# Performance work log

Measured on AMD Instinct MI355X. Metric: run time of the kernel, lower is better.

Reference implementation:

```python
import jax, jax.numpy as jnp
import numpy as np

B, S, D = 2, 2048, 1024
H = 16
HD = D // H  # 64

def setup_inputs() -> dict:
    key = jax.random.key(0)
    k1, k2, k3 = jax.random.split(key, 3)
    scale = 0.02
    return {
        "x": jax.random.normal(k1, (B, S, D), dtype=jnp.float32),
        "w_qkv": jax.random.normal(k2, (D, 3 * D), dtype=jnp.float32) * scale,
        "b_qkv": jnp.zeros((3 * D,), dtype=jnp.float32),
        "w_proj": jax.random.normal(k3, (D, D), dtype=jnp.float32) * scale,
        "b_proj": jnp.zeros((D,), dtype=jnp.float32),
    }

def reference(x, w_qkv, b_qkv, w_proj, b_proj):
    batch, seq_len, _ = x.shape
    qkv = x @ w_qkv + b_qkv                      # [B,S,3D]
    qkv = qkv.reshape(batch, seq_len, 3, H, HD)
    qkv = jnp.transpose(qkv, (2, 0, 3, 1, 4))    # [3,B,H,S,HD]
    q, k, v = qkv[0], qkv[1], qkv[2]
    attn = jnp.einsum('bhqd,bhkd->bhqk', q, k) / jnp.sqrt(jnp.float32(HD))
    attn = jax.nn.softmax(attn, axis=-1)         # [B,H,S,S]
    out = jnp.einsum('bhqk,bhkd->bhqd', attn, v)
    out = jnp.transpose(out, (0, 2, 1, 3)).reshape(batch, seq_len, -1)
    return out @ w_proj + b_proj
```

## Files before the change

### kernel.cpp

```cpp
#include <hip/hip_runtime.h>
#include <math.h>

#define SS 2048
#define DD 1024
#define HH 16
#define NQKV 3072
#define MROWS 4096
#define KD 1024

typedef __attribute__((ext_vector_type(8))) short bf16x8;
typedef __attribute__((ext_vector_type(8))) unsigned short us8;
typedef __attribute__((ext_vector_type(4))) float f32x4;
typedef unsigned short u16;
typedef unsigned int u32;

#define SCALE_C 0.18033688011112042f

#define GLDS16(g, l) \
  __builtin_amdgcn_global_load_lds((const __attribute__((address_space(1))) u32*)(g), \
                                   (__attribute__((address_space(3))) u32*)(l), 16, 0, 0)

static __device__ __forceinline__ u16 f2bf(float f) {
  union { float f; u32 u; } v; v.f = f;
  u32 u = v.u;
  u += 0x7fffu + ((u >> 16) & 1u);
  return (u16)(u >> 16);
}
static __device__ __forceinline__ float bf2f(u16 x) {
  union { u32 u; float f; } v; v.u = ((u32)x) << 16; return v.f;
}
static __device__ __forceinline__ u32 pk2(float a, float b) {
  return (u32)f2bf(a) | ((u32)f2bf(b) << 16);
}
static __device__ __forceinline__ u32 pk2t(float a, float b) {
  union { float f; u32 u; } ua, ub; ua.f = a; ub.f = b;
  return __builtin_amdgcn_perm(ub.u, ua.u, 0x07060302u);
}

__global__ __launch_bounds__(256) void k_prep(const float* __restrict__ x,
                                              const float* __restrict__ w_qkv,
                                              const float* __restrict__ w_proj,
                                              u16* __restrict__ x_bf,
                                              u16* __restrict__ wqkvT,
                                              u16* __restrict__ wprojT) {
  __shared__ float t[64][65];
  int bx = blockIdx.x;
  int tid = threadIdx.x;
  if (bx < 2048) {
    int i = (bx * 256 + tid) * 8;
    float4 a = *(const float4*)(x + i);
    float4 b = *(const float4*)(x + i + 4);
    us8 o;
    o[0] = f2bf(a.x); o[1] = f2bf(a.y); o[2] = f2bf(a.z); o[3] = f2bf(a.w);
    o[4] = f2bf(b.x); o[5] = f2bf(b.y); o[6] = f2bf(b.z); o[7] = f2bf(b.w);
    *(us8*)(x_bf + i) = o;
    return;
  }
  const float* in; u16* out; int R = KD, C, tile;
  if (bx < 2048 + 768) { in = w_qkv; out = wqkvT; C = NQKV; tile = bx - 2048; }
  else                 { in = w_proj; out = wprojT; C = DD; tile = bx - 2816; }
  int tilesC = C >> 6;
  int tc = tile % tilesC, tr = tile / tilesC;
  int r0 = tr * 64, c0 = tc * 64;
  int lx = tid & 63, ly = tid >> 6;
#pragma unroll
  for (int i = 0; i < 16; i++) {
    int rr = ly + i * 4;
    t[rr][lx] = in[(size_t)(r0 + rr) * C + c0 + lx];
  }
  __syncthreads();
#pragma unroll
  for (int i = 0; i < 16; i++) {
    int cc = ly + i * 4;
    out[(size_t)(c0 + cc) * R + r0 + lx] = f2bf(t[lx][cc]);
  }
}

template <int MODE, int BM>
__global__ __launch_bounds__(256, 2) void k_gemm(const u16* __restrict__ A,
                                                 const u16* __restrict__ Bt,
                                                 const float* __restrict__ bias,
                                                 void* __restrict__ Cout,
                                                 u16* __restrict__ vt,
                                                 int M, int N, int K) {
  constexpr int MT = BM / 32;
  __shared__ alignas(16) u16 As[BM * 32];
  __shared__ alignas(16) u16 Bs[128 * 32];
  const int tid = threadIdx.x;
  const int w = tid >> 6, ln = tid & 63;
  const int wm = w >> 1, wn = w & 1;
  const int lm = ln & 15, quad = ln >> 4;
  const int m0 = blockIdx.y * BM, n0 = blockIdx.x * 128;
  const int lr = ln >> 2, c = ln & 3;
  const int cg = c ^ (lr & 3);

  f32x4 acc[MT][4];
#pragma unroll
  for (int i = 0; i < MT; i++)
#pragma unroll
    for (int j = 0; j < 4; j++) acc[i][j] = (f32x4){0.f, 0.f, 0.f, 0.f};

  const u16* gA0 = A  + (size_t)(m0 + 16 * w       + lr) * K + cg * 8;
  const u16* gA1 = A  + (size_t)(m0 + 16 * (w + 4) + lr) * K + cg * 8;
  const u16* gB0 = Bt + (size_t)(n0 + 16 * w       + lr) * K + cg * 8;
  const u16* gB1 = Bt + (size_t)(n0 + 16 * (w + 4) + lr) * K + cg * 8;
  char* lA0 = (char*)As + w * 1024;
  char* lA1 = (char*)As + (w + 4) * 1024;
  char* lB0 = (char*)Bs + w * 1024;
  char* lB1 = (char*)Bs + (w + 4) * 1024;

  for (int k0 = 0; k0 < K; k0 += 32) {
    GLDS16(gA0 + k0, lA0);
    if (BM == 128) GLDS16(gA1 + k0, lA1);
    GLDS16(gB0 + k0, lB0);
    GLDS16(gB1 + k0, lB1);
    __syncthreads();
    bf16x8 af[MT], bfr[4];
#pragma unroll
    for (int t = 0; t < MT; t++)
      af[t]  = *(const bf16x8*)((const char*)As + (wm * (MT * 16) + t * 16 + lm) * 64 + ((quad ^ (lm & 3)) * 16));
#pragma unroll
    for (int t = 0; t < 4; t++)
      bfr[t] = *(const bf16x8*)((const char*)Bs + (wn * 64 + t * 16 + lm) * 64 + ((quad ^ (lm & 3)) * 16));
#pragma unroll
    for (int mt = 0; mt < MT; mt++)
#pragma unroll
      for (int nt = 0; nt < 4; nt++)
        acc[mt][nt] = __builtin_amdgcn_mfma_f32_16x16x32_bf16(af[mt], bfr[nt], acc[mt][nt], 0, 0, 0);
    __syncthreads();
  }

  float bv[4];
#pragma unroll
  for (int nt = 0; nt < 4; nt++) bv[nt] = bias[n0 + wn * 64 + nt * 16 + lm];

  if (MODE == 2 && n0 >= 2 * DD) {
    int b = m0 >> 11;
    int s0 = (m0 & 2047) + wm * 64;
#pragma unroll
    for (int mt = 0; mt < MT; mt++) {
      int s = s0 + mt * 16 + quad * 4;
#pragma unroll
      for (int nt = 0; nt < 4; nt++) {
        int n = n0 + wn * 64 + nt * 16 + lm;
        int bh = b * HH + ((n - 2 * DD) >> 6);
        int d = n & 63;
        uint2 v;
        v.x = pk2(acc[mt][nt][0] + bv[nt], acc[mt][nt][1] + bv[nt]);
        v.y = pk2(acc[mt][nt][2] + bv[nt], acc[mt][nt][3] + bv[nt]);
        *(uint2*)&vt[(size_t)(bh * 64 + d) * SS + s] = v;
      }
    }
    return;
  }

  const float qs = (MODE == 2 && n0 < DD) ? SCALE_C : 1.0f;
#pragma unroll
  for (int mt = 0; mt < MT; mt++) {
#pragma unroll
    for (int r = 0; r < 4; r++) {
      int row = m0 + wm * (MT * 16) + mt * 16 + quad * 4 + r;
#pragma unroll
      for (int nt = 0; nt < 4; nt++) {
        int col = n0 + wn * 64 + nt * 16 + lm;
        float v = (acc[mt][nt][r] + bv[nt]) * qs;
        if (MODE == 2) ((u16*)Cout)[(size_t)row * N + col] = f2bf(v);
        else           ((float*)Cout)[(size_t)row * N + col] = v;
      }
    }
  }
}

__global__ __launch_bounds__(256, 4) void k_attn(const u16* __restrict__ qkv,
                                                 const u16* __restrict__ vt,
                                                 u16* __restrict__ po0,
                                                 u16* __restrict__ po1,
                                                 float* __restrict__ lb0,
                                                 float* __restrict__ lb1) {
  __shared__ alignas(16) u16 Ks[2][64 * 64];
  __shared__ alignas(16) u16 Vs[2][64 * 64];
  __shared__ alignas(16) u16 Ps[4 * 16 * 64];

  const int tid = threadIdx.x;
  const int w = tid >> 6, ln = tid & 63;
  const int lm = ln & 15, quad = ln >> 4;
  const int bx = blockIdx.x;
  const int half = bx >> 9;
  const int bxx = bx & 511;
  const int bh = bxx >> 4;
  const int q0 = (bxx & 15) * 128;
  const int b = bh >> 4, h = bh & 15;
  const size_t qkv_b = (size_t)b * SS * NQKV;
  const int hcol = h * 64;
  const int kvoff = half * (SS / 2);

  u16* __restrict__ po = half ? po1 : po0;
  float* __restrict__ lb = half ? lb1 : lb0;

  const int lr = ln >> 3, cc = ln & 7;
  const int cg = cc ^ lr;

  bf16x8 qf[2][2];
#pragma unroll
  for (int qs2 = 0; qs2 < 2; qs2++)
#pragma unroll
    for (int kk = 0; kk < 2; kk++)
      qf[qs2][kk] = *(const bf16x8*)(qkv + qkv_b +
                     (size_t)(q0 + w * 32 + qs2 * 16 + lm) * NQKV + hcol + kk * 32 + quad * 8);

  f32x4 o[4][2];
  float l[2] = {0.f, 0.f};
#pragma unroll
  for (int t = 0; t < 4; t++) { o[t][0] = (f32x4){0, 0, 0, 0}; o[t][1] = (f32x4){0, 0, 0, 0}; }

  char* psw = (char*)Ps + w * 2048;

#pragma unroll
  for (int rr = 0; rr < 2; rr++) {
    int i = w + 4 * rr;
    GLDS16(qkv + qkv_b + (size_t)(kvoff + 8 * i + lr) * NQKV + DD + hcol + cg * 8, (char*)Ks[0] + i * 1024);
    GLDS16(vt + (size_t)(bh * 64 + 8 * i + lr) * SS + kvoff + cg * 8,              (char*)Vs[0] + i * 1024);
  }

#pragma unroll 1
  for (int it = 0; it < 16; it++) {
    __syncthreads();

    if (it + 1 < 16) {
      int kv1 = kvoff + (it + 1) * 64;
      char* kd = (char*)Ks[(it + 1) & 1];
      char* vd = (char*)Vs[(it + 1) & 1];
#pragma unroll
      for (int rr = 0; rr < 2; rr++) {
        int i = w + 4 * rr;
        GLDS16(qkv + qkv_b + (size_t)(kv1 + 8 * i + lr) * NQKV + DD + hcol + cg * 8, kd + i * 1024);
        GLDS16(vt + (size_t)(bh * 64 + 8 * i + lr) * SS + kv1 + cg * 8,              vd + i * 1024);
      }
    }

    const char* ksb = (const char*)Ks[it & 1];
    const char* vsb = (const char*)Vs[it & 1];

    f32x4 s[4][2];
#pragma unroll
    for (int t = 0; t < 4; t++) { s[t][0] = (f32x4){0, 0, 0, 0}; s[t][1] = (f32x4){0, 0, 0, 0}; }
#pragma unroll
    for (int kk = 0; kk < 2; kk++)
#pragma unroll
      for (int t = 0; t < 4; t++) {
        bf16x8 kf = *(const bf16x8*)(ksb + (t * 16 + lm) * 128 + (((kk * 4 + quad) ^ (lm & 7)) * 16));
        s[t][0] = __builtin_amdgcn_mfma_f32_16x16x32_bf16(kf, qf[0][kk], s[t][0], 0, 0, 0);
        s[t][1] = __builtin_amdgcn_mfma_f32_16x16x32_bf16(kf, qf[1][kk], s[t][1], 0, 0, 0);
      }

    bf16x8 vf[2][4];
#pragma unroll
    for (int kk = 0; kk < 2; kk++)
#pragma unroll
      for (int t = 0; t < 4; t++)
        vf[kk][t] = *(const bf16x8*)(vsb + (t * 16 + lm) * 128 + (((kk * 4 + quad) ^ (lm & 7)) * 16));

#pragma unroll
    for (int qs2 = 0; qs2 < 2; qs2++) {
      float sum = 0.f;
      u32 pkv[4][2];
#pragma unroll
      for (int t = 0; t < 4; t++) {
        float p0 = __builtin_amdgcn_exp2f(s[t][qs2][0]);
        float p1 = __builtin_amdgcn_exp2f(s[t][qs2][1]);
        float p2 = __builtin_amdgcn_exp2f(s[t][qs2][2]);
        float p3 = __builtin_amdgcn_exp2f(s[t][qs2][3]);
        sum += (p0 + p1) + (p2 + p3);
        pkv[t][0] = pk2t(p0, p1);
        pkv[t][1] = pk2t(p2, p3);
      }
      sum += __shfl_xor(sum, 16);
      sum += __shfl_xor(sum, 32);
      l[qs2] += sum;
#pragma unroll
      for (int t = 0; t < 4; t++) {
        uint2 v; v.x = pkv[t][0]; v.y = pkv[t][1];
        *(uint2*)(psw + lm * 128 + (((2 * t + (quad >> 1)) ^ (lm & 7)) * 16) + (quad & 1) * 8) = v;
      }
      bf16x8 pf0 = *(const bf16x8*)(psw + lm * 128 + (((0 + quad) ^ (lm & 7)) * 16));
      bf16x8 pf1 = *(const bf16x8*)(psw + lm * 128 + (((4 + quad) ^ (lm & 7)) * 16));
#pragma unroll
      for (int t = 0; t < 4; t++) {
        o[t][qs2] = __builtin_amdgcn_mfma_f32_16x16x32_bf16(vf[0][t], pf0, o[t][qs2], 0, 0, 0);
        o[t][qs2] = __builtin_amdgcn_mfma_f32_16x16x32_bf16(vf[1][t], pf1, o[t][qs2], 0, 0, 0);
      }
    }
  }

#pragma unroll
  for (int qs2 = 0; qs2 < 2; qs2++) {
    int qg = q0 + w * 32 + qs2 * 16 + lm;
    if (quad == 0) lb[(size_t)bh * SS + qg] = l[qs2];
    int row = b * SS + qg;
#pragma unroll
    for (int t = 0; t < 4; t++) {
      uint2 v;
      v.x = pk2(o[t][qs2][0], o[t][qs2][1]);
      v.y = pk2(o[t][qs2][2], o[t][qs2][3]);
      *(uint2*)&po[(size_t)row * DD + hcol + t * 16 + quad * 4] = v;
    }
  }
}

__global__ __launch_bounds__(256) void k_comb(u16* __restrict__ po0,
                                              const u16* __restrict__ po1,
                                              const float* __restrict__ l0,
                                              const float* __restrict__ l1) {
  int i = (blockIdx.x * 256 + threadIdx.x) * 8;
  int row = i >> 10, col = i & 1023;
  int h = col >> 6, b = row >> 11, q = row & 2047;
  size_t li = (size_t)(b * HH + h) * SS + q;
  float il = 1.0f / (l0[li] + l1[li]);
  us8 a = *(const us8*)(po0 + i);
  us8 p = *(const us8*)(po1 + i);
  us8 o;
#pragma unroll
  for (int j = 0; j < 8; j++) o[j] = f2bf((bf2f(a[j]) + bf2f(p[j])) * il);
  *(us8*)(po0 + i) = o;
}

extern "C" void kernel_launch(void* const* d_in, const int* in_sizes, int n_in,
                              void* d_out, int out_size, void* d_ws, size_t ws_size,
                              hipStream_t stream) {
  const float* x      = (const float*)d_in[0];
  const float* w_qkv  = (const float*)d_in[1];
  const float* b_qkv  = (const float*)d_in[2];
  const float* w_proj = (const float*)d_in[3];
  const float* b_proj = (const float*)d_in[4];
  float* out = (float*)d_out;

  u16* ws     = (u16*)d_ws;
  u16* x_bf   = ws;
  u16* wqkvT  = x_bf   + (size_t)MROWS * KD;
  u16* wprojT = wqkvT  + (size_t)NQKV * KD;
  u16* qkv    = wprojT + (size_t)DD * KD;
  u16* attn   = qkv    + (size_t)MROWS * NQKV;
  u16* vt     = attn   + (size_t)MROWS * DD;

  float* l0 = (float*)wqkvT;
  float* l1 = l0 + (size_t)2 * HH * SS;

  k_prep<<<3072, 256, 0, stream>>>(x, w_qkv, w_proj, x_bf, wqkvT, wprojT);
  k_gemm<2, 128><<<dim3(NQKV / 128, MROWS / 128), 256, 0, stream>>>(x_bf, wqkvT, b_qkv, qkv, vt, MROWS, NQKV, KD);
  k_attn<<<2 * 2 * HH * (SS / 128), 256, 0, stream>>>(qkv, vt, attn, x_bf, l0, l1);
  k_comb<<<(MROWS * DD) / (256 * 8), 256, 0, stream>>>(attn, x_bf, l0, l1);
  k_gemm<0, 64><<<dim3(DD / 128, MROWS / 64), 256, 0, stream>>>(attn, wprojT, b_proj, out, nullptr, MROWS, DD, KD);
}
```

Baseline: 210.0 us.

## Drop split-KV attention with combine kernel; widen GEMM K-tile to 64

New measurement: 186.3 us. -11.3%, faster.

```diff
diff --git a/kernel.cpp b/kernel.cpp
--- a/kernel.cpp
+++ b/kernel.cpp
@@ -25,9 +25,6 @@
   u32 u = v.u;
   u += 0x7fffu + ((u >> 16) & 1u);
   return (u16)(u >> 16);
-}
-static __device__ __forceinline__ float bf2f(u16 x) {
-  union { u32 u; float f; } v; v.u = ((u32)x) << 16; return v.f;
 }
 static __device__ __forceinline__ u32 pk2(float a, float b) {
   return (u32)f2bf(a) | ((u32)f2bf(b) << 16);
@@ -84,15 +81,15 @@
                                                  u16* __restrict__ vt,
                                                  int M, int N, int K) {
   constexpr int MT = BM / 32;
-  __shared__ alignas(16) u16 As[BM * 32];
-  __shared__ alignas(16) u16 Bs[128 * 32];
+  __shared__ alignas(16) u16 As[BM * 64];
+  __shared__ alignas(16) u16 Bs[128 * 64];
   const int tid = threadIdx.x;
   const int w = tid >> 6, ln = tid & 63;
   const int wm = w >> 1, wn = w & 1;
   const int lm = ln & 15, quad = ln >> 4;
   const int m0 = blockIdx.y * BM, n0 = blockIdx.x * 128;
-  const int lr = ln >> 2, c = ln & 3;
-  const int cg = c ^ (lr & 3);
+  const int lr = ln >> 3, cc = ln & 7;
+  const int cg = cc ^ lr;
 
   f32x4 acc[MT][4];
 #pragma unroll
@@ -100,33 +97,41 @@
 #pragma unroll
     for (int j = 0; j < 4; j++) acc[i][j] = (f32x4){0.f, 0.f, 0.f, 0.f};
 
-  const u16* gA0 = A  + (size_t)(m0 + 16 * w       + lr) * K + cg * 8;
-  const u16* gA1 = A  + (size_t)(m0 + 16 * (w + 4) + lr) * K + cg * 8;
-  const u16* gB0 = Bt + (size_t)(n0 + 16 * w       + lr) * K + cg * 8;
-  const u16* gB1 = Bt + (size_t)(n0 + 16 * (w + 4) + lr) * K + cg * 8;
-  char* lA0 = (char*)As + w * 1024;
-  char* lA1 = (char*)As + (w + 4) * 1024;
-  char* lB0 = (char*)Bs + w * 1024;
-  char* lB1 = (char*)Bs + (w + 4) * 1024;
-
-  for (int k0 = 0; k0 < K; k0 += 32) {
-    GLDS16(gA0 + k0, lA0);
-    if (BM == 128) GLDS16(gA1 + k0, lA1);
-    GLDS16(gB0 + k0, lB0);
-    GLDS16(gB1 + k0, lB1);
+  const u16* gA = A  + (size_t)(m0 + lr) * K + cg * 8;
+  const u16* gB = Bt + (size_t)(n0 + lr) * K + cg * 8;
+
+  for (int k0 = 0; k0 < K; k0 += 64) {
+#pragma unroll
+    for (int ii = 0; ii < MT; ii++) {
+      int i = w + 4 * ii;
+      GLDS16(gA + (size_t)(8 * i) * K + k0, (char*)As + i * 1024);
+    }
+#pragma unroll
+    for (int ii = 0; ii < 4; ii++) {
+      int i = w + 4 * ii;
+      GLDS16(gB + (size_t)(8 * i) * K + k0, (char*)Bs + i * 1024);
+    }
     __syncthreads();
-    bf16x8 af[MT], bfr[4];
+    bf16x8 af[MT][2], bfr[4][2];
 #pragma unroll
     for (int t = 0; t < MT; t++)
-      af[t]  = *(const bf16x8*)((const char*)As + (wm * (MT * 16) + t * 16 + lm) * 64 + ((quad ^ (lm & 3)) * 16));
+#pragma unroll
+      for (int kk = 0; kk < 2; kk++)
+        af[t][kk] = *(const bf16x8*)((const char*)As + (wm * (MT * 16) + t * 16 + lm) * 128 +
+                                     (((kk * 4 + quad) ^ (lm & 7)) * 16));
 #pragma unroll
     for (int t = 0; t < 4; t++)
-      bfr[t] = *(const bf16x8*)((const char*)Bs + (wn * 64 + t * 16 + lm) * 64 + ((quad ^ (lm & 3)) * 16));
-#pragma unroll
-    for (int mt = 0; mt < MT; mt++)
-#pragma unroll
-      for (int nt = 0; nt < 4; nt++)
-        acc[mt][nt] = __builtin_amdgcn_mfma_f32_16x16x32_bf16(af[mt], bfr[nt], acc[mt][nt], 0, 0, 0);
+#pragma unroll
+      for (int kk = 0; kk < 2; kk++)
+        bfr[t][kk] = *(const bf16x8*)((const char*)Bs + (wn * 64 + t * 16 + lm) * 128 +
+                                      (((kk * 4 + quad) ^ (lm & 7)) * 16));
+#pragma unroll
+    for (int kk = 0; kk < 2; kk++)
+#pragma unroll
+      for (int mt = 0; mt < MT; mt++)
+#pragma unroll
+        for (int nt = 0; nt < 4; nt++)
+          acc[mt][nt] = __builtin_amdgcn_mfma_f32_16x16x32_bf16(af[mt][kk], bfr[nt][kk], acc[mt][nt], 0, 0, 0);
     __syncthreads();
   }
 
@@ -171,31 +176,22 @@
   }
 }
 
-__global__ __launch_bounds__(256, 4) void k_attn(const u16* __restrict__ qkv,
+__global__ __launch_bounds__(256, 2) void k_attn(const u16* __restrict__ qkv,
                                                  const u16* __restrict__ vt,
-                                                 u16* __restrict__ po0,
-                                                 u16* __restrict__ po1,
-                                                 float* __restrict__ lb0,
-                                                 float* __restrict__ lb1) {
+                                                 u16* __restrict__ attn) {
   __shared__ alignas(16) u16 Ks[2][64 * 64];
   __shared__ alignas(16) u16 Vs[2][64 * 64];
-  __shared__ alignas(16) u16 Ps[4 * 16 * 64];
+  __shared__ alignas(16) u16 Ps[4 * 32 * 64];
 
   const int tid = threadIdx.x;
   const int w = tid >> 6, ln = tid & 63;
   const int lm = ln & 15, quad = ln >> 4;
   const int bx = blockIdx.x;
-  const int half = bx >> 9;
-  const int bxx = bx & 511;
-  const int bh = bxx >> 4;
-  const int q0 = (bxx & 15) * 128;
+  const int bh = bx >> 4;
+  const int q0 = (bx & 15) * 128;
   const int b = bh >> 4, h = bh & 15;
   const size_t qkv_b = (size_t)b * SS * NQKV;
   const int hcol = h * 64;
-  const int kvoff = half * (SS / 2);
-
-  u16* __restrict__ po = half ? po1 : po0;
-  float* __restrict__ lb = half ? lb1 : lb0;
 
   const int lr = ln >> 3, cc = ln & 7;
   const int cg = cc ^ lr;
@@ -213,21 +209,21 @@
 #pragma unroll
   for (int t = 0; t < 4; t++) { o[t][0] = (f32x4){0, 0, 0, 0}; o[t][1] = (f32x4){0, 0, 0, 0}; }
 
-  char* psw = (char*)Ps + w * 2048;
+  char* psw = (char*)Ps + w * 4096;
 
 #pragma unroll
   for (int rr = 0; rr < 2; rr++) {
     int i = w + 4 * rr;
-    GLDS16(qkv + qkv_b + (size_t)(kvoff + 8 * i + lr) * NQKV + DD + hcol + cg * 8, (char*)Ks[0] + i * 1024);
-    GLDS16(vt + (size_t)(bh * 64 + 8 * i + lr) * SS + kvoff + cg * 8,              (char*)Vs[0] + i * 1024);
+    GLDS16(qkv + qkv_b + (size_t)(8 * i + lr) * NQKV + DD + hcol + cg * 8, (char*)Ks[0] + i * 1024);
+    GLDS16(vt + (size_t)(bh * 64 + 8 * i + lr) * SS + cg * 8,              (char*)Vs[0] + i * 1024);
   }
 
 #pragma unroll 1
-  for (int it = 0; it < 16; it++) {
+  for (int it = 0; it < SS / 64; it++) {
     __syncthreads();
 
-    if (it + 1 < 16) {
-      int kv1 = kvoff + (it + 1) * 64;
+    if (it + 1 < SS / 64) {
+      int kv1 = (it + 1) * 64;
       char* kd = (char*)Ks[(it + 1) & 1];
       char* vd = (char*)Vs[(it + 1) & 1];
 #pragma unroll
@@ -280,48 +276,39 @@
 #pragma unroll
       for (int t = 0; t < 4; t++) {
         uint2 v; v.x = pkv[t][0]; v.y = pkv[t][1];
-        *(uint2*)(psw + lm * 128 + (((2 * t + (quad >> 1)) ^ (lm & 7)) * 16) + (quad & 1) * 8) = v;
-      }
-      bf16x8 pf0 = *(const bf16x8*)(psw + lm * 128 + (((0 + quad) ^ (lm & 7)) * 16));
-      bf16x8 pf1 = *(const bf16x8*)(psw + lm * 128 + (((4 + quad) ^ (lm & 7)) * 16));
+        *(uint2*)(psw + (qs2 * 16 + lm) * 128 +
+                  (((2 * t + (quad >> 1)) ^ (lm & 7)) * 16) + (quad & 1) * 8) = v;
+      }
+    }
+
+    bf16x8 pf[2][2];
+#pragma unroll
+    for (int qs2 = 0; qs2 < 2; qs2++)
+#pragma unroll
+      for (int kk = 0; kk < 2; kk++)
+        pf[qs2][kk] = *(const bf16x8*)(psw + (qs2 * 16 + lm) * 128 +
+                                       (((kk * 4 + quad) ^ (lm & 7)) * 16));
+#pragma unroll
+    for (int kk = 0; kk < 2; kk++)
 #pragma unroll
       for (int t = 0; t < 4; t++) {
-        o[t][qs2] = __builtin_amdgcn_mfma_f32_16x16x32_bf16(vf[0][t], pf0, o[t][qs2], 0, 0, 0);
-        o[t][qs2] = __builtin_amdgcn_mfma_f32_16x16x32_bf16(vf[1][t], pf1, o[t][qs2], 0, 0, 0);
-      }
-    }
+        o[t][0] = __builtin_amdgcn_mfma_f32_16x16x32_bf16(vf[kk][t], pf[0][kk], o[t][0], 0, 0, 0);
+        o[t][1] = __builtin_amdgcn_mfma_f32_16x16x32_bf16(vf[kk][t], pf[1][kk], o[t][1], 0, 0, 0);
+      }
   }
 
 #pragma unroll
   for (int qs2 = 0; qs2 < 2; qs2++) {
-    int qg = q0 + w * 32 + qs2 * 16 + lm;
-    if (quad == 0) lb[(size_t)bh * SS + qg] = l[qs2];
-    int row = b * SS + qg;
+    float il = 1.0f / l[qs2];
+    int row = b * SS + q0 + w * 32 + qs2 * 16 + lm;
 #pragma unroll
     for (int t = 0; t < 4; t++) {
       uint2 v;
-      v.x = pk2(o[t][qs2][0], o[t][qs2][1]);
-      v.y = pk2(o[t][qs2][2], o[t][qs2][3]);
-      *(uint2*)&po[(size_t)row * DD + hcol + t * 16 + quad * 4] = v;
-    }
-  }
-}
-
-__global__ __launch_bounds__(256) void k_comb(u16* __restrict__ po0,
-                                              const u16* __restrict__ po1,
-                                              const float* __restrict__ l0,
-                                              const float* __restrict__ l1) {
-  int i = (blockIdx.x * 256 + threadIdx.x) * 8;
-  int row = i >> 10, col = i & 1023;
-  int h = col >> 6, b = row >> 11, q = row & 2047;
-  size_t li = (size_t)(b * HH + h) * SS + q;
-  float il = 1.0f / (l0[li] + l1[li]);
-  us8 a = *(const us8*)(po0 + i);
-  us8 p = *(const us8*)(po1 + i);
-  us8 o;
-#pragma unroll
-  for (int j = 0; j < 8; j++) o[j] = f2bf((bf2f(a[j]) + bf2f(p[j])) * il);
-  *(us8*)(po0 + i) = o;
+      v.x = pk2(o[t][qs2][0] * il, o[t][qs2][1] * il);
+      v.y = pk2(o[t][qs2][2] * il, o[t][qs2][3] * il);
+      *(uint2*)&attn[(size_t)row * DD + hcol + t * 16 + quad * 4] = v;
+    }
+  }
 }
 
 extern "C" void kernel_launch(void* const* d_in, const int* in_sizes, int n_in,
@@ -342,12 +329,8 @@
   u16* attn   = qkv    + (size_t)MROWS * NQKV;
   u16* vt     = attn   + (size_t)MROWS * DD;
 
-  float* l0 = (float*)wqkvT;
-  float* l1 = l0 + (size_t)2 * HH * SS;
-
   k_prep<<<3072, 256, 0, stream>>>(x, w_qkv, w_proj, x_bf, wqkvT, wprojT);
   k_gemm<2, 128><<<dim3(NQKV / 128, MROWS / 128), 256, 0, stream>>>(x_bf, wqkvT, b_qkv, qkv, vt, MROWS, NQKV, KD);
-  k_attn<<<2 * 2 * HH * (SS / 128), 256, 0, stream>>>(qkv, vt, attn, x_bf, l0, l1);
-  k_comb<<<(MROWS * DD) / (256 * 8), 256, 0, stream>>>(attn, x_bf, l0, l1);
+  k_attn<<<2 * HH * (SS / 128), 256, 0, stream>>>(qkv, vt, attn);
   k_gemm<0, 64><<<dim3(DD / 128, MROWS / 64), 256, 0, stream>>>(attn, wprojT, b_proj, out, nullptr, MROWS, DD, KD);
 }
```
